# Kernel tuning notes

Hardware: AMD Instinct MI355X
Metric: run time of the kernel (lower is better)

## Reference

```python
import jax, jax.numpy as jnp
import numpy as np
from jax import lax

NUM_INPUT = 4
NUM_OUTPUT = 1
NUM_U = 10
N = NUM_U // NUM_OUTPUT          # MPC horizon
BATCH = 1024
NINEQ_U = 2 * NUM_U              # input box constraints
NINEQ_X = 2 * NUM_INPUT * N      # soft state constraints
NZ = NUM_U                       # control decision variable dim
NE = NINEQ_X                     # slack variable dim
NW = NZ + NE                     # combined QP variable w = [z; e]
IPM_ITERS = 20                   # fixed-iteration primal-dual interior point
SIGMA = 0.1                      # centering parameter
REG = 1e-8                       # KKT regularization


def setup_inputs():
    key = jax.random.key(0)
    ks = jax.random.split(key, 6)
    x = 0.5 * jax.random.normal(ks[0], (BATCH, NUM_INPUT), dtype=jnp.float32)
    # equality constraint pins z0 = u0; keep inside the |z| <= 0.5 box so QP is feasible
    u0 = (jax.random.uniform(ks[1], (BATCH, NUM_OUTPUT), dtype=jnp.float32) - 0.5) * 0.8
    Q_sqrt = jax.random.uniform(ks[2], (NUM_INPUT, NUM_INPUT), dtype=jnp.float32)
    R_sqrt = jax.random.uniform(ks[3], (NUM_OUTPUT, NUM_OUTPUT), dtype=jnp.float32)
    # scale A so that A^N stays bounded (torch init rand() would blow up at N=10)
    A_dyn = 0.3 * jax.random.uniform(ks[4], (NUM_INPUT, NUM_INPUT), dtype=jnp.float32)
    B_dyn = jax.random.uniform(ks[5], (NUM_INPUT, NUM_OUTPUT), dtype=jnp.float32)
    return {"x": x, "u0": u0, "Q_sqrt": Q_sqrt, "R_sqrt": R_sqrt,
            "A_dyn": A_dyn, "B_dyn": B_dyn}


def _build_mpc_blocks(A, B):
    # A_hat = [A; A^2; ...; A^N],  B_hat = lower block-Toeplitz of A^k B
    Apows = [A]
    for _ in range(1, N):
        Apows.append(Apows[-1] @ A)
    A_hat = jnp.concatenate(Apows, axis=0)                 # (N*n, n)
    T = [B]
    for _ in range(1, N):
        T.append(A @ T[-1])
    T = jnp.stack(T)                                        # (N, n, m), T[k] = A^k B
    i = jnp.arange(N)
    diff = i[:, None] - i[None, :]
    blocks = jnp.where((diff >= 0)[:, :, None, None],
                       T[jnp.clip(diff, 0, N - 1)], 0.0)    # (N, N, n, m)
    B_hat = blocks.transpose(0, 2, 1, 3).reshape(N * NUM_INPUT, N * NUM_OUTPUT)
    return A_hat, B_hat


def _max_step(v, dv):
    # largest alpha keeping v + alpha*dv > 0 (per batch row)
    ratio = jnp.where(dv < -1e-12, -v / jnp.minimum(dv, -1e-12), 1e8)
    return jnp.min(ratio, axis=-1, keepdims=True)


def _qp_solve(H, q, G, h, Aeq, beq):
    # min 0.5 w^T H w + q^T w  s.t. G w <= h, Aeq w = beq
    # H, G, Aeq shared; q, h, beq batched. Infeasible-start primal-dual IPM.
    b, nw = q.shape
    mI = G.shape[0]
    ne = Aeq.shape[0]
    w = jnp.zeros((b, nw), q.dtype)
    nu = jnp.zeros((b, ne), q.dtype)
    s = jnp.maximum(h, 1.0)
    lam = jnp.ones((b, mI), q.dtype)
    I_nw = jnp.eye(nw, dtype=q.dtype)
    I_ne = jnp.eye(ne, dtype=q.dtype)

    def step(carry, _):
        w, s, lam, nu = carry
        Gw = w @ G.T
        r_dual = w @ H + q + lam @ G + nu @ Aeq            # (b, nw)
        r_prim = Gw + s - h                                # (b, mI)
        r_eq = w @ Aeq.T - beq                             # (b, ne)
        mu = SIGMA * jnp.sum(s * lam, axis=-1, keepdims=True) / mI
        d = lam / s
        tmp = (mu - lam * s + lam * r_prim) / s
        rw = -(r_dual + tmp @ G)
        rn = -r_eq
        # Schur complement in w: M = H + G^T diag(lam/s) G
        M = H[None] + (G.T[None, :, :] * d[:, None, :]) @ G + REG * I_nw
        AeqT = jnp.broadcast_to(Aeq.T[None], (b, nw, ne))
        AeqB = jnp.broadcast_to(Aeq[None], (b, ne, nw))
        corner = jnp.broadcast_to((-REG * I_ne)[None], (b, ne, ne))
        K = jnp.concatenate([jnp.concatenate([M, AeqT], axis=2),
                             jnp.concatenate([AeqB, corner], axis=2)], axis=1)
        rhs = jnp.concatenate([rw, rn], axis=1)
        sol = jnp.linalg.solve(K, rhs[..., None])[..., 0]
        dw, dnu = sol[:, :nw], sol[:, nw:]
        ds = -(dw @ G.T) - r_prim
        dlam = (mu - lam * s - lam * ds) / s
        alpha = 0.99 * jnp.minimum(1.0, jnp.minimum(_max_step(s, ds),
                                                    _max_step(lam, dlam)))
        return (w + alpha * dw, s + alpha * ds,
                lam + alpha * dlam, nu + alpha * dnu), None

    (w, s, lam, nu), _ = lax.scan(step, (w, s, lam, nu), None, length=IPM_ITERS)
    return w


def _forward(x, u0, Q_sqrt, R_sqrt, A_dyn, B_dyn):
    b = x.shape[0]
    dt = x.dtype
    x0 = x.reshape(b, -1)
    A_hat, B_hat = _build_mpc_blocks(A_dyn, B_dyn)
    Q = Q_sqrt @ Q_sqrt.T
    R = R_sqrt @ R_sqrt.T
    Q_diag = jnp.kron(jnp.eye(N, dtype=dt), Q)   # block-diag(Q,...,Q,P) with P = Q
    R_diag = jnp.kron(jnp.eye(N, dtype=dt), R)
    Q_hat = B_hat.T @ (Q_diag @ B_hat) + R_diag  # (nz, nz)
    A_x0 = x0 @ A_hat.T                           # (b, n*N)
    p = 2.0 * A_x0 @ (Q_diag @ B_hat)             # (b, nz)
    G1 = jnp.concatenate([jnp.eye(NZ, dtype=dt), -jnp.eye(NZ, dtype=dt)], axis=0)
    G2 = jnp.concatenate([B_hat, -B_hat], axis=0)
    h1 = 0.5 * jnp.ones((b, NINEQ_U), dt)
    h21 = 4.0 * jnp.ones((b, NUM_INPUT * N), dt) - A_x0
    h22 = 4.0 * jnp.ones((b, NUM_INPUT * N), dt) + A_x0
    h2 = jnp.concatenate([h21, h22], axis=1)
    E = jnp.eye(NE, dtype=dt)                     # E_sqrt = I so E = I
    # combined QP over w = [z; e]:
    #   min z^T Q_hat z + p^T z + e^T E e
    #   s.t. G1 z <= h1, G2 z - e <= h2, -e <= 0, F z = f
    # (sum_squares(sqrtm(Q_hat) z) == z^T Q_hat z, so sqrtm cancels exactly)
    H = 2.0 * jnp.block([[Q_hat, jnp.zeros((NZ, NE), dt)],
                         [jnp.zeros((NE, NZ), dt), E]])
    q = jnp.concatenate([p, jnp.zeros((b, NE), dt)], axis=1)
    Ie = jnp.eye(NE, dtype=dt)
    G_all = jnp.concatenate([
        jnp.concatenate([G1, jnp.zeros((NINEQ_U, NE), dt)], axis=1),
        jnp.concatenate([G2, -Ie], axis=1),
        jnp.concatenate([jnp.zeros((NE, NZ), dt), -Ie], axis=1)], axis=0)
    h_all = jnp.concatenate([h1, h2, jnp.zeros((b, NE), dt)], axis=1)
    F = jnp.zeros((1, NW), dt).at[0, 0].set(1.0)  # F z = f with F = e_0^T (padded over e)
    beq = u0.reshape(b, -1)
    w = _qp_solve(H, q, G_all, h_all, F, beq)
    u_opt = w[:, :NZ]
    e_opt = w[:, NZ:]
    a = jnp.sum((u_opt @ Q_hat) * u_opt + p * u_opt, axis=1)
    bterm = jnp.sum((A_x0 @ Q_diag) * A_x0, axis=1)
    c = jnp.sum((x0 @ Q) * x0, axis=1)
    dterm = jnp.sum((e_opt @ E) * e_opt, axis=1)
    cost_opt = (a + bterm + c + dterm)[:, None]
    u0_opt = u_opt[:, 0]   # weight vector is e_0
    return cost_opt, u0_opt


def reference(x, u0, Q_sqrt, R_sqrt, A_dyn, B_dyn):
    return _forward(x, u0, Q_sqrt, R_sqrt, A_dyn, B_dyn)
```

## Files before the change

### kernel.cpp

```cpp
#include <hip/hip_runtime.h>

#define BATCH 1024
#define ITERS 20
#define SIGMA_C 0.1f
#define REG_C 1e-8f

typedef float f2 __attribute__((ext_vector_type(2)));

__device__ __forceinline__ float frcp(float x) { return __builtin_amdgcn_rcpf(x); }
__device__ __forceinline__ float readlane_f(float v, int l) {
    return __int_as_float(__builtin_amdgcn_readlane(__float_as_int(v), l));
}
__device__ __forceinline__ f2 mkf2(float a, float b) { f2 r; r.x = a; r.y = b; return r; }
__device__ __forceinline__ f2 fma2(f2 a, f2 b, f2 c) { return a * b + c; }

#define WFENCE() do { __builtin_amdgcn_wave_barrier(); asm volatile("" ::: "memory"); } while (0)

#define DPPF(v, ctrl) \
    __int_as_float(__builtin_amdgcn_update_dpp(0, __float_as_int(v), ctrl, 0xf, 0xf, true))

__device__ __forceinline__ float wave_sum(float v) {
    v += DPPF(v, 0xB1);
    v += DPPF(v, 0x4E);
    v += DPPF(v, 0x141);
    v += DPPF(v, 0x140);
    v += __shfl_xor(v, 16);
    v += __shfl_xor(v, 32);
    return v;
}

#define RED3_DPP(ctrl) do { \
    p1 += DPPF(p1, ctrl); \
    p2 += DPPF(p2, ctrl); \
    q = fmaxf(q, DPPF(q, ctrl)); \
} while (0)

__global__ __launch_bounds__(64, 1) void ipm_kernel(
    const float* __restrict__ x, const float* __restrict__ u0p,
    const float* __restrict__ Qs, const float* __restrict__ Rs,
    const float* __restrict__ Ad, const float* __restrict__ Bd,
    float* __restrict__ out)
{
    const int item = blockIdx.x;
    const int lane = threadIdx.x;

    __shared__ __align__(16) float BLc[10 * 40];
    __shared__ __align__(16) float QBc[10 * 40];
    __shared__ __align__(16) float yL4[40];
    __shared__ __align__(16) float QhL[10 * 12];
    __shared__ __align__(16) float SL[10 * 12];
    __shared__ __align__(16) float cg[80];
    __shared__ float duL[20], ltL[20];
    __shared__ float axL[40];
    __shared__ float pvL[10], wL[10];
    __shared__ float QL[16];
    __shared__ float TL[40];
    __shared__ float AhL[160];

    const int r2 = (lane >> 2) & 3, c2 = lane & 3;
    const int r4 = lane & 3;

    if (lane < 16) {
        float acc = 0.f;
        #pragma unroll
        for (int k = 0; k < 4; ++k) acc += Qs[r2 * 4 + k] * Qs[c2 * 4 + k];
        QL[lane] = acc;
    }

    float acol[4];
    #pragma unroll
    for (int k = 0; k < 4; ++k) acol[k] = Ad[k * 4 + c2];
    float cur = Ad[r2 * 4 + c2];
    if (lane < 16) AhL[r2 * 4 + c2] = cur;
    #pragma unroll
    for (int i = 1; i < 10; ++i) {
        float nx = 0.f;
        #pragma unroll
        for (int k = 0; k < 4; ++k) nx += __shfl(cur, r2 * 4 + k) * acol[k];
        cur = nx;
        if (lane < 16) AhL[(4 * i + r2) * 4 + c2] = cur;
    }

    float arow[4];
    #pragma unroll
    for (int k = 0; k < 4; ++k) arow[k] = Ad[r4 * 4 + k];
    float tc = Bd[r4];
    if (lane < 4) TL[r4] = tc;
    #pragma unroll
    for (int i = 1; i < 10; ++i) {
        float nt = 0.f;
        #pragma unroll
        for (int k = 0; k < 4; ++k) nt += arow[k] * __shfl(tc, k);
        tc = nt;
        if (lane < 4) TL[i * 4 + r4] = nt;
    }
    __syncthreads();

    const int kk40 = (lane < 40) ? lane : 39;
    const int ib = lane >> 2;
    float b[10];
    #pragma unroll
    for (int j = 0; j < 10; ++j) {
        int dd = ib - j;
        int dc = dd < 0 ? 0 : (dd > 9 ? 9 : dd);
        float v = TL[dc * 4 + r4];
        b[j] = (dd >= 0 && lane < 40) ? v : 0.f;
    }

    const float xv0 = x[item * 4 + 0], xv1 = x[item * 4 + 1];
    const float xv2 = x[item * 4 + 2], xv3 = x[item * 4 + 3];
    const float ax = AhL[kk40 * 4 + 0] * xv0 + AhL[kk40 * 4 + 1] * xv1 +
                     AhL[kk40 * 4 + 2] * xv2 + AhL[kk40 * 4 + 3] * xv3;
    if (lane < 40) axL[lane] = ax;

    const int gbase = lane & ~3;
    float yv = 0.f;
    #pragma unroll
    for (int rp_ = 0; rp_ < 4; ++rp_) yv += QL[r4 * 4 + rp_] * __shfl(ax, gbase + rp_);
    if (lane < 40) yL4[lane] = yv;
    #pragma unroll
    for (int cc = 0; cc < 10; ++cc) {
        float acc = 0.f;
        #pragma unroll
        for (int rp_ = 0; rp_ < 4; ++rp_) acc += QL[r4 * 4 + rp_] * __shfl(b[cc], gbase + rp_);
        if (lane < 40) QBc[cc * 40 + lane] = acc;
    }
    if (lane < 40) {
        #pragma unroll
        for (int j = 0; j < 10; ++j) BLc[j * 40 + lane] = b[j];
    }
    __syncthreads();

    if (lane < 10) {
        const float4* br = reinterpret_cast<const float4*>(&BLc[lane * 40]);
        const float4* yy = reinterpret_cast<const float4*>(yL4);
        float acc = 0.f;
        #pragma unroll
        for (int i = 0; i < 10; ++i) {
            const float4 a_ = br[i], b_ = yy[i];
            acc += a_.x * b_.x + a_.y * b_.y + a_.z * b_.z + a_.w * b_.w;
        }
        pvL[lane] = 2.f * acc;
    }
    const float R2v = Rs[0] * Rs[0];
    #pragma unroll
    for (int p = 0; p < 2; ++p) {
        const int t = lane + 64 * p;
        if (t < 100) {
            const int aa = t / 10, bb = t - aa * 10;
            const float4* ba = reinterpret_cast<const float4*>(&BLc[aa * 40]);
            const float4* qb = reinterpret_cast<const float4*>(&QBc[bb * 40]);
            float acc = (aa == bb) ? R2v : 0.f;
            #pragma unroll
            for (int i = 0; i < 10; ++i) {
                const float4 a_ = ba[i], b_ = qb[i];
                acc += a_.x * b_.x + a_.y * b_.y + a_.z * b_.z + a_.w * b_.w;
            }
            QhL[aa * 12 + bb] = acc;
        }
    }
    __syncthreads();

    const bool rLane = (lane < 10);
    const bool sLane = (lane >= 10 && lane < 60);
    const int t1 = sLane ? 2 * (lane - 10) : 0;
    const int srow = t1 / 10, sc1 = t1 - srow * 10, sc2 = sc1 + 1;
    f2 tA[20], tB[20];
    float qh_a = 0.f, qh_b = 0.f;
    bool diagA = false, diagB = false;
    if (sLane) {
        const float4* br = reinterpret_cast<const float4*>(&BLc[srow * 40]);
        const float4* b1 = reinterpret_cast<const float4*>(&BLc[sc1 * 40]);
        const float4* b2 = reinterpret_cast<const float4*>(&BLc[sc2 * 40]);
        #pragma unroll
        for (int i = 0; i < 10; ++i) {
            const float4 r_ = br[i], u_ = b1[i], v_ = b2[i];
            tA[2*i]   = mkf2(r_.x * u_.x, r_.y * u_.y);
            tA[2*i+1] = mkf2(r_.z * u_.z, r_.w * u_.w);
            tB[2*i]   = mkf2(r_.x * v_.x, r_.y * v_.y);
            tB[2*i+1] = mkf2(r_.z * v_.z, r_.w * v_.w);
        }
        qh_a = 2.f * QhL[srow * 12 + sc1];
        qh_b = 2.f * QhL[srow * 12 + sc2];
        diagA = (srow == sc1); diagB = (srow == sc2);
    } else if (rLane) {
        const float4* br = reinterpret_cast<const float4*>(&BLc[lane * 40]);
        #pragma unroll
        for (int i = 0; i < 10; ++i) {
            const float4 r_ = br[i];
            tA[2*i]   = mkf2(r_.x, r_.y);
            tA[2*i+1] = mkf2(r_.z, r_.w);
        }
        #pragma unroll
        for (int c = 0; c < 5; ++c)
            tB[c] = mkf2(QhL[lane * 12 + 2*c], QhL[lane * 12 + 2*c + 1]);
        qh_a = pvL[lane];
    }
    __syncthreads();

    float s_B = fmaxf(4.f - ax, 1.f), s_C = fmaxf(4.f + ax, 1.f);
    float s_D = 1.f, s_E = 1.f, s_U = 1.f;
    float l_B = 1.f, l_C = 1.f, l_D = 1.f, l_E = 1.f, l_U = 1.f;
    float w2a = 0.f, w2b = 0.f;
    float w1[10];
    #pragma unroll
    for (int r = 0; r < 10; ++r) w1[r] = 0.f;
    float w1own = 0.f, nu = 0.f;
    const float uu0 = u0p[item];
    const bool a40 = lane < 40, a20 = lane < 20;
    const int jown = (lane < 10) ? lane : lane - 10;
    const float sgnU = (lane < 10) ? 1.f : -1.f;

    float mu;
    {
        float part = a40 ? (s_B * l_B + s_C * l_C + s_D * l_D + s_E * l_E) : 0.f;
        if (a20) part += s_U * l_U;
        mu = SIGMA_C * wave_sum(part) * (1.f / 180.f);
    }

    for (int it = 0; it < ITERS; ++it) {
        const float rs_B = frcp(s_B), rs_C = frcp(s_C), rs_D = frcp(s_D),
                    rs_E = frcp(s_E), rs_U = frcp(s_U);
        const float rl_B = frcp(l_B), rl_C = frcp(l_C), rl_D = frcp(l_D),
                    rl_E = frcp(l_E), rl_U = frcp(l_U);
        const float d_B = l_B * rs_B, d_C = l_C * rs_C, d_D = l_D * rs_D,
                    d_E = l_E * rs_E, d_U = l_U * rs_U;

        f2 bu = mkf2(0.f, 0.f);
        #pragma unroll
        for (int j = 0; j < 5; ++j)
            bu = fma2(mkf2(b[2*j], b[2*j+1]), mkf2(w1[2*j], w1[2*j+1]), bu);
        const float Bu = bu.x + bu.y;

        const float rp_B = Bu - w2a + s_B - (4.f - ax);
        const float rp_C = -Bu - w2b + s_C - (4.f + ax);
        const float rp_D = -w2a + s_D;
        const float rp_E = -w2b + s_E;
        const float rp_U = sgnU * w1own + s_U - 0.5f;

        const float tm_B = (mu - l_B * s_B + l_B * rp_B) * rs_B;
        const float tm_C = (mu - l_C * s_C + l_C * rp_C) * rs_C;
        const float tm_D = (mu - l_D * s_D + l_D * rp_D) * rs_D;
        const float tm_E = (mu - l_E * s_E + l_E * rp_E) * rs_E;
        const float tm_U = (mu - l_U * s_U + l_U * rp_U) * rs_U;
        const float lt_B = l_B + tm_B, lt_C = l_C + tm_C, lt_D = l_D + tm_D,
                    lt_E = l_E + tm_E;

        const float D22a = 2.f + d_B + d_D + REG_C, D22b = 2.f + d_C + d_E + REG_C;
        const float rda = frcp(D22a), rdb = frcp(D22b);
        const float rw2a = -2.f * w2a + lt_B + lt_D;
        const float rw2b = -2.f * w2b + lt_C + lt_E;
        const float coeff = (d_B + d_C) - d_B * d_B * rda - d_C * d_C * rdb;
        const float gvc = (d_B * rw2a * rda - d_C * rw2b * rdb) - (lt_B - lt_C);

        if (a40) { cg[lane] = coeff; cg[40 + lane] = gvc; }
        if (a20) { duL[lane] = d_U; ltL[lane] = l_U + tm_U; }
        WFENCE();

        float4 cf4[10];
        {
            const float4* cp = reinterpret_cast<const float4*>(cg + (rLane ? 40 : 0));
            #pragma unroll
            for (int i = 0; i < 10; ++i) cf4[i] = cp[i];
        }

        float p0 = a40 ? (s_B * l_B + s_C * l_C + s_D * l_D + s_E * l_E) : 0.f;
        if (a20) p0 += s_U * l_U;
        p0 = wave_sum(p0);

        float rhs_loc = 0.f;
        if (sLane) {
            f2 aA0 = mkf2(0.f, 0.f), aA1 = mkf2(0.f, 0.f);
            f2 aB0 = mkf2(0.f, 0.f), aB1 = mkf2(0.f, 0.f);
            #pragma unroll
            for (int i = 0; i < 10; ++i) {
                const f2 cl = mkf2(cf4[i].x, cf4[i].y);
                const f2 ch = mkf2(cf4[i].z, cf4[i].w);
                aA0 = fma2(tA[2*i], cl, aA0); aA1 = fma2(tA[2*i+1], ch, aA1);
                aB0 = fma2(tB[2*i], cl, aB0); aB1 = fma2(tB[2*i+1], ch, aB1);
            }
            float vA = ((aA0.x + aA0.y) + (aA1.x + aA1.y)) + qh_a;
            float vB = ((aB0.x + aB0.y) + (aB1.x + aB1.y)) + qh_b;
            if (diagA || diagB) {
                const float dd = duL[srow] + duL[10 + srow] + REG_C;
                if (diagA) vA += dd; else vB += dd;
            }
            *reinterpret_cast<float2*>(&SL[srow * 12 + sc1]) = make_float2(vA, vB);
        } else if (rLane) {
            f2 a0 = mkf2(0.f, 0.f), a1 = mkf2(0.f, 0.f);
            #pragma unroll
            for (int i = 0; i < 10; ++i) {
                const f2 cl = mkf2(cf4[i].x, cf4[i].y);
                const f2 ch = mkf2(cf4[i].z, cf4[i].w);
                a0 = fma2(tA[2*i], cl, a0); a1 = fma2(tA[2*i+1], ch, a1);
            }
            const float acc = (a0.x + a0.y) + (a1.x + a1.y);
            f2 qa = mkf2(0.f, 0.f);
            #pragma unroll
            for (int c = 0; c < 5; ++c)
                qa = fma2(tB[c], mkf2(w1[2*c], w1[2*c+1]), qa);
            const float qw = qa.x + qa.y;
            rhs_loc = acc - (2.f * qw + qh_a + ltL[lane] - ltL[10 + lane] +
                             ((lane == 0) ? nu : 0.f));
        }
        WFENCE();

        float row[11], rBv;
        if (rLane) {
            const float4* s4 = reinterpret_cast<const float4*>(&SL[lane * 12]);
            const float4 q0 = s4[0], q1 = s4[1], q2 = s4[2];
            row[0] = q0.x; row[1] = q0.y; row[2] = q0.z; row[3] = q0.w;
            row[4] = q1.x; row[5] = q1.y; row[6] = q1.z; row[7] = q1.w;
            row[8] = q2.x; row[9] = q2.y;
            (void)q2;
        } else {
            #pragma unroll
            for (int c = 0; c < 10; ++c) row[c] = 0.f;
        }
        row[10] = rhs_loc;
        rBv = (lane == 0) ? 1.f : 0.f;

        #pragma unroll
        for (int kc = 0; kc < 9; ++kc) {
            float pk[11];
            #pragma unroll
            for (int c = kc; c < 11; ++c) pk[c] = readlane_f(row[c], kc);
            const float pB = readlane_f(rBv, kc);
            const float rpiv = frcp(pk[kc]);
            const float f = (lane > kc) ? row[kc] * rpiv : 0.f;
            #pragma unroll
            for (int c = kc + 1; c < 11; ++c) row[c] -= f * pk[c];
            rBv -= f * pB;
        }

        float rd[10];
        #pragma unroll
        for (int r = 0; r < 10; ++r) rd[r] = frcp(row[r]);

        float dwAv[10], dwBv[10], ownA = 0.f, ownB = 0.f;
        #pragma unroll
        for (int r = 9; r >= 0; --r) {
            const float bA = readlane_f(row[10] * rd[r], r);
            const float bB = readlane_f(rBv * rd[r], r);
            dwAv[r] = bA; dwBv[r] = bB;
            if (jown == r) { ownA = bA; ownB = bB; }
            const float m_ = (lane < r) ? 1.f : 0.f;
            row[10] -= m_ * row[r] * bA;
            rBv     -= m_ * row[r] * bB;
        }

        const float rn = -(w1[0] - uu0);
        const float nu_d = (dwAv[0] - rn) * frcp(dwBv[0] + REG_C);
        float dw1[10];
        #pragma unroll
        for (int r = 0; r < 10; ++r) dw1[r] = dwAv[r] - nu_d * dwBv[r];
        const float dOwn = ownA - nu_d * ownB;

        f2 bd = mkf2(0.f, 0.f);
        #pragma unroll
        for (int j = 0; j < 5; ++j)
            bd = fma2(mkf2(b[2*j], b[2*j+1]), mkf2(dw1[2*j], dw1[2*j+1]), bd);
        const float Bdw = bd.x + bd.y;

        const float dw2a = (rw2a + d_B * Bdw) * rda;
        const float dw2b = (rw2b - d_C * Bdw) * rdb;

        const float ds_B = -(Bdw - dw2a) - rp_B;
        const float ds_C = (Bdw + dw2b) - rp_C;
        const float ds_D = dw2a - rp_D;
        const float ds_E = dw2b - rp_E;
        const float ds_U = -sgnU * dOwn - rp_U;
        const float dl_B = (mu - l_B * s_B - l_B * ds_B) * rs_B;
        const float dl_C = (mu - l_C * s_C - l_C * ds_C) * rs_C;
        const float dl_D = (mu - l_D * s_D - l_D * ds_D) * rs_D;
        const float dl_E = (mu - l_E * s_E - l_E * ds_E) * rs_E;
        const float dl_U = (mu - l_U * s_U - l_U * ds_U) * rs_U;

        float q = 0.f, p1 = 0.f, p2 = 0.f;
        if (a40) {
            q = fmaxf(q, (ds_B < -1e-12f) ? -ds_B * rs_B : 0.f);
            q = fmaxf(q, (ds_C < -1e-12f) ? -ds_C * rs_C : 0.f);
            q = fmaxf(q, (ds_D < -1e-12f) ? -ds_D * rs_D : 0.f);
            q = fmaxf(q, (ds_E < -1e-12f) ? -ds_E * rs_E : 0.f);
            q = fmaxf(q, (dl_B < -1e-12f) ? -dl_B * rl_B : 0.f);
            q = fmaxf(q, (dl_C < -1e-12f) ? -dl_C * rl_C : 0.f);
            q = fmaxf(q, (dl_D < -1e-12f) ? -dl_D * rl_D : 0.f);
            q = fmaxf(q, (dl_E < -1e-12f) ? -dl_E * rl_E : 0.f);
            p1 = (s_B * dl_B + l_B * ds_B) + (s_C * dl_C + l_C * ds_C) +
                 (s_D * dl_D + l_D * ds_D) + (s_E * dl_E + l_E * ds_E);
            p2 = ds_B * dl_B + ds_C * dl_C + ds_D * dl_D + ds_E * dl_E;
        }
        if (a20) {
            q = fmaxf(q, (ds_U < -1e-12f) ? -ds_U * rs_U : 0.f);
            q = fmaxf(q, (dl_U < -1e-12f) ? -dl_U * rl_U : 0.f);
            p1 += s_U * dl_U + l_U * ds_U;
            p2 += ds_U * dl_U;
        }
        RED3_DPP(0xB1);
        RED3_DPP(0x4E);
        RED3_DPP(0x141);
        RED3_DPP(0x140);
        p1 += __shfl_xor(p1, 16); p2 += __shfl_xor(p2, 16);
        q = fmaxf(q, __shfl_xor(q, 16));
        p1 += __shfl_xor(p1, 32); p2 += __shfl_xor(p2, 32);
        q = fmaxf(q, __shfl_xor(q, 32));

        const float alpha = 0.99f * ((q > 1.f) ? frcp(q) : 1.f);
        mu = SIGMA_C * (p0 + alpha * (p1 + alpha * p2)) * (1.f / 180.f);

        s_B += alpha * ds_B; s_C += alpha * ds_C; s_D += alpha * ds_D;
        s_E += alpha * ds_E; s_U += alpha * ds_U;
        l_B += alpha * dl_B; l_C += alpha * dl_C; l_D += alpha * dl_D;
        l_E += alpha * dl_E; l_U += alpha * dl_U;
        w2a += alpha * dw2a; w2b += alpha * dw2b;
        #pragma unroll
        for (int r = 0; r < 10; ++r) w1[r] += alpha * dw1[r];
        w1own += alpha * dOwn;
        nu += alpha * nu_d;
        WFENCE();
    }

    if (lane == 0) {
        #pragma unroll
        for (int r = 0; r < 10; ++r) wL[r] = w1[r];
    }
    __syncthreads();
    float part = a40 ? (w2a * w2a + w2b * w2b) : 0.f;
    for (int idx = lane; idx < 100; idx += 64) {
        const int r = idx / 10, c = idx - r * 10;
        part += wL[r] * QhL[r * 12 + c] * wL[c];
    }
    if (lane < 10) part += pvL[lane] * wL[lane];
    for (int idx = lane; idx < 160; idx += 64) {
        const int i2 = idx >> 4, rc = idx & 15, rr2 = rc >> 2, cc2 = rc & 3;
        part += axL[i2 * 4 + rr2] * QL[rc] * axL[i2 * 4 + cc2];
    }
    if (lane == 0) {
        float ct = 0.f;
        #pragma unroll
        for (int r = 0; r < 4; ++r) {
            const float xr = (r == 0 ? xv0 : r == 1 ? xv1 : r == 2 ? xv2 : xv3);
            #pragma unroll
            for (int c = 0; c < 4; ++c) {
                const float xc = (c == 0 ? xv0 : c == 1 ? xv1 : c == 2 ? xv2 : xv3);
                ct += xr * QL[r * 4 + c] * xc;
            }
        }
        part += ct;
    }
    const float cost = wave_sum(part);
    if (lane == 0) {
        out[item] = cost;
        out[BATCH + item] = w1[0];
    }
}

extern "C" void kernel_launch(void* const* d_in, const int* in_sizes, int n_in,
                              void* d_out, int out_size, void* d_ws, size_t ws_size,
                              hipStream_t stream) {
    const float* x  = (const float*)d_in[0];
    const float* u0 = (const float*)d_in[1];
    const float* Qs = (const float*)d_in[2];
    const float* Rs = (const float*)d_in[3];
    const float* Ad = (const float*)d_in[4];
    const float* Bd = (const float*)d_in[5];
    float* outp = (float*)d_out;
    ipm_kernel<<<dim3(BATCH), dim3(64), 0, stream>>>(x, u0, Qs, Rs, Ad, Bd, outp);
}
```

Before: 99.72 us.

## Update Bu and Q·w incrementally, use DPP row-broadcast reductions, precompute pivot reciprocals

The Bu and Q·w1 products are now kept as running values, updated each iteration with alpha times the products of the step direction, so the separate dot products over w1 are no longer recomputed. The wave reductions swap the cross-row shfl_xor steps for DPP row_bcast15/31 followed by a readlane from lane 63. The Gaussian elimination computes each pivot reciprocal per lane right after the row update and broadcasts it, which removes the trailing reciprocal loop from the elimination's critical path. The incremental updates can drift slightly in floating point compared with recomputing the products directly.

```diff
diff --git a/kernel.cpp b/kernel.cpp
--- a/kernel.cpp
+++ b/kernel.cpp
@@ -18,6 +18,8 @@
 
 #define DPPF(v, ctrl) \
     __int_as_float(__builtin_amdgcn_update_dpp(0, __float_as_int(v), ctrl, 0xf, 0xf, true))
+#define DPPB(v, ctrl, rmask) \
+    __int_as_float(__builtin_amdgcn_update_dpp(0, __float_as_int(v), ctrl, rmask, 0xf, false))
 
 __device__ __forceinline__ float wave_sum(float v) {
     v += DPPF(v, 0xB1);
@@ -206,6 +208,8 @@
     #pragma unroll
     for (int r = 0; r < 10; ++r) w1[r] = 0.f;
     float w1own = 0.f, nu = 0.f;
+    float Bu = 0.f;
+    float qwr = 0.f;
     const float uu0 = u0p[item];
     const bool a40 = lane < 40, a20 = lane < 20;
     const int jown = (lane < 10) ? lane : lane - 10;
@@ -226,12 +230,6 @@
         const float d_B = l_B * rs_B, d_C = l_C * rs_C, d_D = l_D * rs_D,
                     d_E = l_E * rs_E, d_U = l_U * rs_U;
 
-        f2 bu = mkf2(0.f, 0.f);
-        #pragma unroll
-        for (int j = 0; j < 5; ++j)
-            bu = fma2(mkf2(b[2*j], b[2*j+1]), mkf2(w1[2*j], w1[2*j+1]), bu);
-        const float Bu = bu.x + bu.y;
-
         const float rp_B = Bu - w2a + s_B - (4.f - ax);
         const float rp_C = -Bu - w2b + s_C - (4.f + ax);
         const float rp_D = -w2a + s_D;
@@ -266,7 +264,13 @@
 
         float p0 = a40 ? (s_B * l_B + s_C * l_C + s_D * l_D + s_E * l_E) : 0.f;
         if (a20) p0 += s_U * l_U;
-        p0 = wave_sum(p0);
+        p0 += DPPF(p0, 0xB1);
+        p0 += DPPF(p0, 0x4E);
+        p0 += DPPF(p0, 0x141);
+        p0 += DPPF(p0, 0x140);
+        p0 += DPPB(p0, 0x142, 0xA);
+        p0 += DPPB(p0, 0x143, 0xC);
+        const float p0T = readlane_f(p0, 63);
 
         float rhs_loc = 0.f;
         if (sLane) {
@@ -295,12 +299,7 @@
                 a0 = fma2(tA[2*i], cl, a0); a1 = fma2(tA[2*i+1], ch, a1);
             }
             const float acc = (a0.x + a0.y) + (a1.x + a1.y);
-            f2 qa = mkf2(0.f, 0.f);
-            #pragma unroll
-            for (int c = 0; c < 5; ++c)
-                qa = fma2(tB[c], mkf2(w1[2*c], w1[2*c+1]), qa);
-            const float qw = qa.x + qa.y;
-            rhs_loc = acc - (2.f * qw + qh_a + ltL[lane] - ltL[10 + lane] +
+            rhs_loc = acc - (2.f * qwr + qh_a + ltL[lane] - ltL[10 + lane] +
                              ((lane == 0) ? nu : 0.f));
         }
         WFENCE();
@@ -312,7 +311,6 @@
             row[0] = q0.x; row[1] = q0.y; row[2] = q0.z; row[3] = q0.w;
             row[4] = q1.x; row[5] = q1.y; row[6] = q1.z; row[7] = q1.w;
             row[8] = q2.x; row[9] = q2.y;
-            (void)q2;
         } else {
             #pragma unroll
             for (int c = 0; c < 10; ++c) row[c] = 0.f;
@@ -320,22 +318,21 @@
         row[10] = rhs_loc;
         rBv = (lane == 0) ? 1.f : 0.f;
 
+        float rd[10];
+        rd[0] = frcp(row[0]);
         #pragma unroll
         for (int kc = 0; kc < 9; ++kc) {
             float pk[11];
             #pragma unroll
-            for (int c = kc; c < 11; ++c) pk[c] = readlane_f(row[c], kc);
+            for (int c = kc + 1; c < 11; ++c) pk[c] = readlane_f(row[c], kc);
             const float pB = readlane_f(rBv, kc);
-            const float rpiv = frcp(pk[kc]);
+            const float rpiv = readlane_f(rd[kc], kc);
             const float f = (lane > kc) ? row[kc] * rpiv : 0.f;
             #pragma unroll
             for (int c = kc + 1; c < 11; ++c) row[c] -= f * pk[c];
             rBv -= f * pB;
-        }
-
-        float rd[10];
-        #pragma unroll
-        for (int r = 0; r < 10; ++r) rd[r] = frcp(row[r]);
+            rd[kc + 1] = frcp(row[kc + 1]);
+        }
 
         float dwAv[10], dwBv[10], ownA = 0.f, ownB = 0.f;
         #pragma unroll
@@ -356,11 +353,15 @@
         for (int r = 0; r < 10; ++r) dw1[r] = dwAv[r] - nu_d * dwBv[r];
         const float dOwn = ownA - nu_d * ownB;
 
-        f2 bd = mkf2(0.f, 0.f);
-        #pragma unroll
-        for (int j = 0; j < 5; ++j)
-            bd = fma2(mkf2(b[2*j], b[2*j+1]), mkf2(dw1[2*j], dw1[2*j+1]), bd);
+        f2 bd = mkf2(0.f, 0.f), qd = mkf2(0.f, 0.f);
+        #pragma unroll
+        for (int j = 0; j < 5; ++j) {
+            const f2 dv = mkf2(dw1[2*j], dw1[2*j+1]);
+            bd = fma2(mkf2(b[2*j], b[2*j+1]), dv, bd);
+            qd = fma2(tB[j], dv, qd);
+        }
         const float Bdw = bd.x + bd.y;
+        const float qdw = qd.x + qd.y;
 
         const float dw2a = (rw2a + d_B * Bdw) * rda;
         const float dw2b = (rw2b - d_C * Bdw) * rdb;
@@ -400,13 +401,16 @@
         RED3_DPP(0x4E);
         RED3_DPP(0x141);
         RED3_DPP(0x140);
-        p1 += __shfl_xor(p1, 16); p2 += __shfl_xor(p2, 16);
-        q = fmaxf(q, __shfl_xor(q, 16));
-        p1 += __shfl_xor(p1, 32); p2 += __shfl_xor(p2, 32);
-        q = fmaxf(q, __shfl_xor(q, 32));
-
-        const float alpha = 0.99f * ((q > 1.f) ? frcp(q) : 1.f);
-        mu = SIGMA_C * (p0 + alpha * (p1 + alpha * p2)) * (1.f / 180.f);
+        p1 += DPPB(p1, 0x142, 0xA); p2 += DPPB(p2, 0x142, 0xA);
+        q = fmaxf(q, DPPB(q, 0x142, 0xA));
+        p1 += DPPB(p1, 0x143, 0xC); p2 += DPPB(p2, 0x143, 0xC);
+        q = fmaxf(q, DPPB(q, 0x143, 0xC));
+        const float qT  = readlane_f(q, 63);
+        const float p1T = readlane_f(p1, 63);
+        const float p2T = readlane_f(p2, 63);
+
+        const float alpha = 0.99f * frcp(fmaxf(qT, 1.f));
+        mu = SIGMA_C * (p0T + alpha * (p1T + alpha * p2T)) * (1.f / 180.f);
 
         s_B += alpha * ds_B; s_C += alpha * ds_C; s_D += alpha * ds_D;
         s_E += alpha * ds_E; s_U += alpha * ds_U;
@@ -417,6 +421,8 @@
         for (int r = 0; r < 10; ++r) w1[r] += alpha * dw1[r];
         w1own += alpha * dOwn;
         nu += alpha * nu_d;
+        Bu  += alpha * Bdw;
+        qwr += alpha * qdw;
         WFENCE();
     }
 
```

After: 97.40 us. -2.3%, faster.
